# Optimization experiments

Measured on AMD Instinct MI355X. Metric: run time of the kernel, lower is better.

Reference implementation:

```python
import jax, jax.numpy as jnp
import numpy as np

NUM_PROCS = 16
PROC_DIM = 8
SPATIAL_DIM = 3
NUM_LOCS = 500000
NAUG = NUM_PROCS * NUM_LOCS  # 8M augmented rows


def setup_inputs() -> dict:
    key = jax.random.key(0)
    k1, k2, k3, k4 = jax.random.split(key, 4)
    proc_pos = jax.random.normal(k1, (NUM_PROCS, PROC_DIM), dtype=jnp.float32)
    locs_sp = jax.random.normal(k2, (NUM_LOCS, SPATIAL_DIM), dtype=jnp.float32)
    process_ids = jax.random.randint(k3, (NAUG,), 0, NUM_PROCS, dtype=jnp.int64)
    location_ids = jax.random.randint(k4, (NAUG,), 0, NUM_LOCS, dtype=jnp.int64)
    return {
        "proc_pos": proc_pos,
        "locs_sp": locs_sp,
        "process_ids": process_ids,
        "location_ids": location_ids,
    }


def reference(proc_pos, locs_sp, process_ids, location_ids):
    # Fused gather-concat: equivalent to the per-row loop of
    # concat([proc_pos[pid], locs_sp[lid]]) stacked over all augmented rows.
    # [NAUG, PROC_DIM] and [NAUG, SPATIAL_DIM] gathers, then concat on feature axis.
    proc_part = jnp.take(proc_pos, process_ids, axis=0)
    loc_part = jnp.take(locs_sp, location_ids, axis=0)
    locs_augmented = jnp.concatenate([proc_part, loc_part], axis=1)  # [NAUG, PROC_DIM+SPATIAL_DIM]
    return locs_augmented
```

## Files before the change

kernel.cpp:

```cpp
#include <hip/hip_runtime.h>
#include <hip/hip_bf16.h>

#define NUM_PROCS 16
#define PROC_DIM 8
#define SPATIAL_DIM 3
#define ROW_DIM (PROC_DIM + SPATIAL_DIM)
#define BLOCK 256
#define RPT 2
#define ROWS_PER_BLOCK (BLOCK * RPT)

typedef float v4f __attribute__((ext_vector_type(4)));
typedef int   v2i __attribute__((ext_vector_type(2)));

__global__ __launch_bounds__(BLOCK) void gather_concat_kernel(
    const float* __restrict__ proc_pos,
    const float* __restrict__ locs_sp,
    const int*   __restrict__ process_ids,
    const int*   __restrict__ location_ids,
    float* __restrict__ out,
    int naug)
{
    __shared__ float sproc[NUM_PROCS * PROC_DIM];
    __shared__ float s[ROWS_PER_BLOCK * ROW_DIM];

    const int t = threadIdx.x;
    const int block_row0 = blockIdx.x * ROWS_PER_BLOCK;
    const bool full = (block_row0 + ROWS_PER_BLOCK <= naug);

    if (t < NUM_PROCS * PROC_DIM) sproc[t] = proc_pos[t];

    const int r0 = block_row0 + 2 * t;
    v2i pid2, lid2;
    if (full) {
        pid2 = __builtin_nontemporal_load((const v2i*)(process_ids + block_row0) + t);
        lid2 = __builtin_nontemporal_load((const v2i*)(location_ids + block_row0) + t);
    } else {
        pid2.x = (r0     < naug) ? process_ids[r0]     : 0;
        pid2.y = (r0 + 1 < naug) ? process_ids[r0 + 1] : 0;
        lid2.x = (r0     < naug) ? location_ids[r0]     : 0;
        lid2.y = (r0 + 1 < naug) ? location_ids[r0 + 1] : 0;
    }

    const float* lp0 = locs_sp + (size_t)lid2.x * SPATIAL_DIM;
    const float* lp1 = locs_sp + (size_t)lid2.y * SPATIAL_DIM;
    float a0 = lp0[0], a1 = lp0[1], a2 = lp0[2];
    float b0 = lp1[0], b1 = lp1[1], b2 = lp1[2];

    __syncthreads();

    const v4f* pp0 = (const v4f*)(sproc + pid2.x * PROC_DIM);
    const v4f* pp1 = (const v4f*)(sproc + pid2.y * PROC_DIM);
    v4f p00 = pp0[0], p01 = pp0[1];
    v4f p10 = pp1[0], p11 = pp1[1];

    float* d0 = s + (size_t)(2 * t) * ROW_DIM;
    d0[0] = p00.x; d0[1] = p00.y; d0[2] = p00.z; d0[3] = p00.w;
    d0[4] = p01.x; d0[5] = p01.y; d0[6] = p01.z; d0[7] = p01.w;
    d0[8] = a0;    d0[9] = a1;    d0[10] = a2;
    float* d1 = d0 + ROW_DIM;
    d1[0] = p10.x; d1[1] = p10.y; d1[2] = p10.z; d1[3] = p10.w;
    d1[4] = p11.x; d1[5] = p11.y; d1[6] = p11.z; d1[7] = p11.w;
    d1[8] = b0;    d1[9] = b1;    d1[10] = b2;

    __syncthreads();

    const v4f* s4 = (const v4f*)s;
    if (full) {
        v4f* out4 = (v4f*)(out + (size_t)block_row0 * ROW_DIM);
        #pragma unroll
        for (int k = 0; k < (ROWS_PER_BLOCK * ROW_DIM) / 4 / BLOCK; ++k) {
            const int i = t + k * BLOCK;
            __builtin_nontemporal_store(s4[i], out4 + i);
        }
        const int i = t + ((ROWS_PER_BLOCK * ROW_DIM) / 4 / BLOCK) * BLOCK;
        if (i < (ROWS_PER_BLOCK * ROW_DIM) / 4) {
            __builtin_nontemporal_store(s4[i], out4 + i);
        }
    } else {
        const int total_f = (naug - block_row0) * ROW_DIM;
        float* outf = out + (size_t)block_row0 * ROW_DIM;
        for (int i = t; i < total_f; i += BLOCK) {
            outf[i] = s[i];
        }
    }
}

extern "C" void kernel_launch(void* const* d_in, const int* in_sizes, int n_in,
                              void* d_out, int out_size, void* d_ws, size_t ws_size,
                              hipStream_t stream) {
    const float* proc_pos     = (const float*)d_in[0];
    const float* locs_sp      = (const float*)d_in[1];
    const int*   process_ids  = (const int*)d_in[2];
    const int*   location_ids = (const int*)d_in[3];
    float* out = (float*)d_out;

    const int naug = in_sizes[2];
    const int grid = (naug + ROWS_PER_BLOCK - 1) / ROWS_PER_BLOCK;

    gather_concat_kernel<<<grid, BLOCK, 0, stream>>>(
        proc_pos, locs_sp, process_ids, location_ids, out, naug);
}
```

Before: 449.0 us.

## Pack four rows per thread into direct vector stores, dropping shared staging

Each thread now handles four consecutive rows. Four rows span 44 floats, which is exactly eleven 16-byte vectors, so the thread writes its output with 11 nontemporal v4 stores straight from registers. This removes the shared-memory staging buffer and one barrier, and it loads the ids as v4i. The proc table is padded to a stride of 12 in LDS to spread bank accesses. The cost is that each lane's stores are strided by 176 bytes instead of being contiguous across the wavefront, which may hurt write coalescing. The block size is halved.

```diff
diff --git a/kernel.cpp b/kernel.cpp
--- a/kernel.cpp
+++ b/kernel.cpp
@@ -1,16 +1,16 @@
 #include <hip/hip_runtime.h>
-#include <hip/hip_bf16.h>
 
 #define NUM_PROCS 16
 #define PROC_DIM 8
 #define SPATIAL_DIM 3
 #define ROW_DIM (PROC_DIM + SPATIAL_DIM)
-#define BLOCK 256
-#define RPT 2
+#define BLOCK 128
+#define RPT 4
 #define ROWS_PER_BLOCK (BLOCK * RPT)
+#define SPROC_STRIDE 12
 
 typedef float v4f __attribute__((ext_vector_type(4)));
-typedef int   v2i __attribute__((ext_vector_type(2)));
+typedef int   v4i __attribute__((ext_vector_type(4)));
 
 __global__ __launch_bounds__(BLOCK) void gather_concat_kernel(
     const float* __restrict__ proc_pos,
@@ -20,67 +20,80 @@
     float* __restrict__ out,
     int naug)
 {
-    __shared__ float sproc[NUM_PROCS * PROC_DIM];
-    __shared__ float s[ROWS_PER_BLOCK * ROW_DIM];
+    __shared__ float sproc[NUM_PROCS * SPROC_STRIDE];
 
     const int t = threadIdx.x;
     const int block_row0 = blockIdx.x * ROWS_PER_BLOCK;
     const bool full = (block_row0 + ROWS_PER_BLOCK <= naug);
 
-    if (t < NUM_PROCS * PROC_DIM) sproc[t] = proc_pos[t];
-
-    const int r0 = block_row0 + 2 * t;
-    v2i pid2, lid2;
-    if (full) {
-        pid2 = __builtin_nontemporal_load((const v2i*)(process_ids + block_row0) + t);
-        lid2 = __builtin_nontemporal_load((const v2i*)(location_ids + block_row0) + t);
-    } else {
-        pid2.x = (r0     < naug) ? process_ids[r0]     : 0;
-        pid2.y = (r0 + 1 < naug) ? process_ids[r0 + 1] : 0;
-        lid2.x = (r0     < naug) ? location_ids[r0]     : 0;
-        lid2.y = (r0 + 1 < naug) ? location_ids[r0 + 1] : 0;
+    if (t < NUM_PROCS * PROC_DIM) {
+        sproc[(t >> 3) * SPROC_STRIDE + (t & 7)] = proc_pos[t];
     }
 
-    const float* lp0 = locs_sp + (size_t)lid2.x * SPATIAL_DIM;
-    const float* lp1 = locs_sp + (size_t)lid2.y * SPATIAL_DIM;
-    float a0 = lp0[0], a1 = lp0[1], a2 = lp0[2];
-    float b0 = lp1[0], b1 = lp1[1], b2 = lp1[2];
+    const int r0 = block_row0 + RPT * t;
 
-    __syncthreads();
+    if (full) {
+        v4i pid4 = __builtin_nontemporal_load((const v4i*)(process_ids + block_row0) + t);
+        v4i lid4 = __builtin_nontemporal_load((const v4i*)(location_ids + block_row0) + t);
 
-    const v4f* pp0 = (const v4f*)(sproc + pid2.x * PROC_DIM);
-    const v4f* pp1 = (const v4f*)(sproc + pid2.y * PROC_DIM);
-    v4f p00 = pp0[0], p01 = pp0[1];
-    v4f p10 = pp1[0], p11 = pp1[1];
+        const float* l0 = locs_sp + (size_t)lid4.x * SPATIAL_DIM;
+        const float* l1 = locs_sp + (size_t)lid4.y * SPATIAL_DIM;
+        const float* l2 = locs_sp + (size_t)lid4.z * SPATIAL_DIM;
+        const float* l3 = locs_sp + (size_t)lid4.w * SPATIAL_DIM;
+        float a0 = l0[0], a1 = l0[1], a2 = l0[2];
+        float b0 = l1[0], b1 = l1[1], b2 = l1[2];
+        float c0 = l2[0], c1 = l2[1], c2 = l2[2];
+        float e0 = l3[0], e1 = l3[1], e2 = l3[2];
 
-    float* d0 = s + (size_t)(2 * t) * ROW_DIM;
-    d0[0] = p00.x; d0[1] = p00.y; d0[2] = p00.z; d0[3] = p00.w;
-    d0[4] = p01.x; d0[5] = p01.y; d0[6] = p01.z; d0[7] = p01.w;
-    d0[8] = a0;    d0[9] = a1;    d0[10] = a2;
-    float* d1 = d0 + ROW_DIM;
-    d1[0] = p10.x; d1[1] = p10.y; d1[2] = p10.z; d1[3] = p10.w;
-    d1[4] = p11.x; d1[5] = p11.y; d1[6] = p11.z; d1[7] = p11.w;
-    d1[8] = b0;    d1[9] = b1;    d1[10] = b2;
+        __syncthreads();
 
-    __syncthreads();
+        const v4f* P0 = (const v4f*)(sproc + pid4.x * SPROC_STRIDE);
+        const v4f* P1 = (const v4f*)(sproc + pid4.y * SPROC_STRIDE);
+        const v4f* P2 = (const v4f*)(sproc + pid4.z * SPROC_STRIDE);
+        const v4f* P3 = (const v4f*)(sproc + pid4.w * SPROC_STRIDE);
+        v4f p0a = P0[0], p0b = P0[1];
+        v4f p1a = P1[0], p1b = P1[1];
+        v4f p2a = P2[0], p2b = P2[1];
+        v4f p3a = P3[0], p3b = P3[1];
 
-    const v4f* s4 = (const v4f*)s;
-    if (full) {
-        v4f* out4 = (v4f*)(out + (size_t)block_row0 * ROW_DIM);
-        #pragma unroll
-        for (int k = 0; k < (ROWS_PER_BLOCK * ROW_DIM) / 4 / BLOCK; ++k) {
-            const int i = t + k * BLOCK;
-            __builtin_nontemporal_store(s4[i], out4 + i);
-        }
-        const int i = t + ((ROWS_PER_BLOCK * ROW_DIM) / 4 / BLOCK) * BLOCK;
-        if (i < (ROWS_PER_BLOCK * ROW_DIM) / 4) {
-            __builtin_nontemporal_store(s4[i], out4 + i);
-        }
+        v4f w0  = {p0a.x, p0a.y, p0a.z, p0a.w};
+        v4f w1  = {p0b.x, p0b.y, p0b.z, p0b.w};
+        v4f w2  = {a0,    a1,    a2,    p1a.x};
+        v4f w3  = {p1a.y, p1a.z, p1a.w, p1b.x};
+        v4f w4  = {p1b.y, p1b.z, p1b.w, b0   };
+        v4f w5  = {b1,    b2,    p2a.x, p2a.y};
+        v4f w6  = {p2a.z, p2a.w, p2b.x, p2b.y};
+        v4f w7  = {p2b.z, p2b.w, c0,    c1   };
+        v4f w8  = {c2,    p3a.x, p3a.y, p3a.z};
+        v4f w9  = {p3a.w, p3b.x, p3b.y, p3b.z};
+        v4f w10 = {p3b.w, e0,    e1,    e2   };
+
+        v4f* o = (v4f*)(out + (size_t)r0 * ROW_DIM);
+        __builtin_nontemporal_store(w0,  o + 0);
+        __builtin_nontemporal_store(w1,  o + 1);
+        __builtin_nontemporal_store(w2,  o + 2);
+        __builtin_nontemporal_store(w3,  o + 3);
+        __builtin_nontemporal_store(w4,  o + 4);
+        __builtin_nontemporal_store(w5,  o + 5);
+        __builtin_nontemporal_store(w6,  o + 6);
+        __builtin_nontemporal_store(w7,  o + 7);
+        __builtin_nontemporal_store(w8,  o + 8);
+        __builtin_nontemporal_store(w9,  o + 9);
+        __builtin_nontemporal_store(w10, o + 10);
     } else {
-        const int total_f = (naug - block_row0) * ROW_DIM;
-        float* outf = out + (size_t)block_row0 * ROW_DIM;
-        for (int i = t; i < total_f; i += BLOCK) {
-            outf[i] = s[i];
+        __syncthreads();
+        for (int k = 0; k < RPT; ++k) {
+            const int r = r0 + k;
+            if (r < naug) {
+                const int pid = process_ids[r];
+                const int lid = location_ids[r];
+                const float* ps = sproc + pid * SPROC_STRIDE;
+                const float* ls = locs_sp + (size_t)lid * SPATIAL_DIM;
+                float* orow = out + (size_t)r * ROW_DIM;
+                #pragma unroll
+                for (int j = 0; j < PROC_DIM; ++j) orow[j] = ps[j];
+                orow[8] = ls[0]; orow[9] = ls[1]; orow[10] = ls[2];
+            }
         }
     }
 }
```

Result: slower. 1.275 ms (+184.1%).

## Use persistent per-wave tiles with software-pipelined index and gather prefetch

Applied to the files above, without the earlier changes.

Replaces the one-tile-per-block launch with a fixed grid of persistent blocks. Each wave owns its own LDS staging tile, so block-wide barriers are no longer needed inside the loop. Index loads are prefetched two tiles ahead and location gathers one tile ahead to hide global memory latency. The proc table is also padded to a 12-float stride to spread LDS bank access, and leftover rows are handled by a single wave. The cost is more register pressure and a serial tail path.

```diff
diff --git a/kernel.cpp b/kernel.cpp
--- a/kernel.cpp
+++ b/kernel.cpp
@@ -1,13 +1,15 @@
 #include <hip/hip_runtime.h>
-#include <hip/hip_bf16.h>
 
 #define NUM_PROCS 16
 #define PROC_DIM 8
 #define SPATIAL_DIM 3
 #define ROW_DIM (PROC_DIM + SPATIAL_DIM)
 #define BLOCK 256
+#define WAVES_PB (BLOCK / 64)
 #define RPT 2
-#define ROWS_PER_BLOCK (BLOCK * RPT)
+#define TROWS (64 * RPT)
+#define TILE_F (TROWS * ROW_DIM)
+#define SPROC_STRIDE 12
 
 typedef float v4f __attribute__((ext_vector_type(4)));
 typedef int   v2i __attribute__((ext_vector_type(2)));
@@ -20,67 +22,103 @@
     float* __restrict__ out,
     int naug)
 {
-    __shared__ float sproc[NUM_PROCS * PROC_DIM];
-    __shared__ float s[ROWS_PER_BLOCK * ROW_DIM];
+    __shared__ float sproc[NUM_PROCS * SPROC_STRIDE];
+    __shared__ float stage[WAVES_PB][TILE_F];
 
-    const int t = threadIdx.x;
-    const int block_row0 = blockIdx.x * ROWS_PER_BLOCK;
-    const bool full = (block_row0 + ROWS_PER_BLOCK <= naug);
+    const int t    = threadIdx.x;
+    const int wv   = t >> 6;
+    const int lane = t & 63;
 
-    if (t < NUM_PROCS * PROC_DIM) sproc[t] = proc_pos[t];
+    if (t < NUM_PROCS * PROC_DIM)
+        sproc[(t >> 3) * SPROC_STRIDE + (t & 7)] = proc_pos[t];
+    __syncthreads();
 
-    const int r0 = block_row0 + 2 * t;
-    v2i pid2, lid2;
-    if (full) {
-        pid2 = __builtin_nontemporal_load((const v2i*)(process_ids + block_row0) + t);
-        lid2 = __builtin_nontemporal_load((const v2i*)(location_ids + block_row0) + t);
-    } else {
-        pid2.x = (r0     < naug) ? process_ids[r0]     : 0;
-        pid2.y = (r0 + 1 < naug) ? process_ids[r0 + 1] : 0;
-        lid2.x = (r0     < naug) ? location_ids[r0]     : 0;
-        lid2.y = (r0 + 1 < naug) ? location_ids[r0 + 1] : 0;
+    const int WT = naug / TROWS;
+    const int gw = blockIdx.x * WAVES_PB + wv;
+    const int NW = gridDim.x * WAVES_PB;
+
+    float* const sl      = stage[wv];
+    const v4f* const s4  = (const v4f*)sl;
+
+    v2i pidC = {0, 0}, lidC = {0, 0};
+    v2i pidN = {0, 0}, lidN = {0, 0};
+    float ca0=0, ca1=0, ca2=0, cb0=0, cb1=0, cb2=0;
+
+    const int wt0 = gw;
+    const int wt1 = gw + NW;
+    if (wt0 < WT) {
+        pidC = __builtin_nontemporal_load((const v2i*)(process_ids + (size_t)wt0 * TROWS) + lane);
+        lidC = __builtin_nontemporal_load((const v2i*)(location_ids + (size_t)wt0 * TROWS) + lane);
+    }
+    if (wt1 < WT) {
+        pidN = __builtin_nontemporal_load((const v2i*)(process_ids + (size_t)wt1 * TROWS) + lane);
+        lidN = __builtin_nontemporal_load((const v2i*)(location_ids + (size_t)wt1 * TROWS) + lane);
+    }
+    if (wt0 < WT) {
+        const float* l0 = locs_sp + (size_t)lidC.x * SPATIAL_DIM;
+        const float* l1 = locs_sp + (size_t)lidC.y * SPATIAL_DIM;
+        ca0 = l0[0]; ca1 = l0[1]; ca2 = l0[2];
+        cb0 = l1[0]; cb1 = l1[1]; cb2 = l1[2];
     }
 
-    const float* lp0 = locs_sp + (size_t)lid2.x * SPATIAL_DIM;
-    const float* lp1 = locs_sp + (size_t)lid2.y * SPATIAL_DIM;
-    float a0 = lp0[0], a1 = lp0[1], a2 = lp0[2];
-    float b0 = lp1[0], b1 = lp1[1], b2 = lp1[2];
+    for (int wt = wt0; wt < WT; wt += NW) {
+        const int wtn  = wt + NW;
+        const int wtnn = wt + 2 * NW;
 
-    __syncthreads();
+        v2i pidT = {0, 0}, lidT = {0, 0};
+        if (wtnn < WT) {
+            pidT = __builtin_nontemporal_load((const v2i*)(process_ids + (size_t)wtnn * TROWS) + lane);
+            lidT = __builtin_nontemporal_load((const v2i*)(location_ids + (size_t)wtnn * TROWS) + lane);
+        }
 
-    const v4f* pp0 = (const v4f*)(sproc + pid2.x * PROC_DIM);
-    const v4f* pp1 = (const v4f*)(sproc + pid2.y * PROC_DIM);
-    v4f p00 = pp0[0], p01 = pp0[1];
-    v4f p10 = pp1[0], p11 = pp1[1];
+        float na0=0, na1=0, na2=0, nb0=0, nb1=0, nb2=0;
+        if (wtn < WT) {
+            const float* l0 = locs_sp + (size_t)lidN.x * SPATIAL_DIM;
+            const float* l1 = locs_sp + (size_t)lidN.y * SPATIAL_DIM;
+            na0 = l0[0]; na1 = l0[1]; na2 = l0[2];
+            nb0 = l1[0]; nb1 = l1[1]; nb2 = l1[2];
+        }
 
-    float* d0 = s + (size_t)(2 * t) * ROW_DIM;
-    d0[0] = p00.x; d0[1] = p00.y; d0[2] = p00.z; d0[3] = p00.w;
-    d0[4] = p01.x; d0[5] = p01.y; d0[6] = p01.z; d0[7] = p01.w;
-    d0[8] = a0;    d0[9] = a1;    d0[10] = a2;
-    float* d1 = d0 + ROW_DIM;
-    d1[0] = p10.x; d1[1] = p10.y; d1[2] = p10.z; d1[3] = p10.w;
-    d1[4] = p11.x; d1[5] = p11.y; d1[6] = p11.z; d1[7] = p11.w;
-    d1[8] = b0;    d1[9] = b1;    d1[10] = b2;
+        const v4f* P0 = (const v4f*)(sproc + pidC.x * SPROC_STRIDE);
+        const v4f* P1 = (const v4f*)(sproc + pidC.y * SPROC_STRIDE);
+        v4f p00 = P0[0], p01 = P0[1];
+        v4f p10 = P1[0], p11 = P1[1];
+        float* d0 = sl + (size_t)(2 * lane) * ROW_DIM;
+        d0[0] = p00.x; d0[1] = p00.y; d0[2]  = p00.z; d0[3] = p00.w;
+        d0[4] = p01.x; d0[5] = p01.y; d0[6]  = p01.z; d0[7] = p01.w;
+        d0[8] = ca0;   d0[9] = ca1;   d0[10] = ca2;
+        float* d1 = d0 + ROW_DIM;
+        d1[0] = p10.x; d1[1] = p10.y; d1[2]  = p10.z; d1[3] = p10.w;
+        d1[4] = p11.x; d1[5] = p11.y; d1[6]  = p11.z; d1[7] = p11.w;
+        d1[8] = cb0;   d1[9] = cb1;   d1[10] = cb2;
 
-    __syncthreads();
-
-    const v4f* s4 = (const v4f*)s;
-    if (full) {
-        v4f* out4 = (v4f*)(out + (size_t)block_row0 * ROW_DIM);
+        v4f* out4 = (v4f*)(out + (size_t)wt * TILE_F);
         #pragma unroll
-        for (int k = 0; k < (ROWS_PER_BLOCK * ROW_DIM) / 4 / BLOCK; ++k) {
-            const int i = t + k * BLOCK;
+        for (int k = 0; k < 5; ++k) {
+            const int i = lane + k * 64;
             __builtin_nontemporal_store(s4[i], out4 + i);
         }
-        const int i = t + ((ROWS_PER_BLOCK * ROW_DIM) / 4 / BLOCK) * BLOCK;
-        if (i < (ROWS_PER_BLOCK * ROW_DIM) / 4) {
+        if (lane < 32) {
+            const int i = 320 + lane;
             __builtin_nontemporal_store(s4[i], out4 + i);
         }
-    } else {
-        const int total_f = (naug - block_row0) * ROW_DIM;
-        float* outf = out + (size_t)block_row0 * ROW_DIM;
-        for (int i = t; i < total_f; i += BLOCK) {
-            outf[i] = s[i];
+
+        pidC = pidN; lidC = lidN; pidN = pidT; lidN = lidT;
+        ca0 = na0; ca1 = na1; ca2 = na2;
+        cb0 = nb0; cb1 = nb1; cb2 = nb2;
+    }
+
+    const int tail0 = WT * TROWS;
+    if (gw == 0) {
+        for (int r = tail0 + lane; r < naug; r += 64) {
+            const int pid = process_ids[r];
+            const int lid = location_ids[r];
+            const float* ps = sproc + pid * SPROC_STRIDE;
+            const float* ls = locs_sp + (size_t)lid * SPATIAL_DIM;
+            float* orow = out + (size_t)r * ROW_DIM;
+            #pragma unroll
+            for (int j = 0; j < PROC_DIM; ++j) orow[j] = ps[j];
+            orow[8] = ls[0]; orow[9] = ls[1]; orow[10] = ls[2];
         }
     }
 }
@@ -95,7 +133,11 @@
     float* out = (float*)d_out;
 
     const int naug = in_sizes[2];
-    const int grid = (naug + ROWS_PER_BLOCK - 1) / ROWS_PER_BLOCK;
+    const int WT   = naug / TROWS;
+
+    int grid = 1792;
+    if (grid * WAVES_PB > WT) grid = (WT + WAVES_PB - 1) / WAVES_PB;
+    if (grid < 1) grid = 1;
 
     gather_concat_kernel<<<grid, BLOCK, 0, stream>>>(
         proc_pos, locs_sp, process_ids, location_ids, out, naug);
```

New measurement: 461.2 us. 1.03x slower.

## Pad location table to float4 in workspace and gather with vector loads

Applied to the files above, without the earlier changes.

Adds a pre-pass kernel that copies the 3-float location table into a 16-byte-stride padded table in the workspace. The main kernel then reads each location with one 128-bit load instead of three scalar loads. The shared-memory proc table stride also changes to 12 floats, apparently to spread LDS bank accesses. The cost is an extra kernel launch that reads and writes about 8 MB each call, and N_LOCS is hardcoded rather than taken from the input sizes.

```diff
diff --git a/kernel.cpp b/kernel.cpp
--- a/kernel.cpp
+++ b/kernel.cpp
@@ -1,5 +1,4 @@
 #include <hip/hip_runtime.h>
-#include <hip/hip_bf16.h>
 
 #define NUM_PROCS 16
 #define PROC_DIM 8
@@ -8,26 +7,42 @@
 #define BLOCK 256
 #define RPT 2
 #define ROWS_PER_BLOCK (BLOCK * RPT)
+#define SPROC_STRIDE 12
+#define N_LOCS 500000
 
 typedef float v4f __attribute__((ext_vector_type(4)));
 typedef int   v2i __attribute__((ext_vector_type(2)));
 
+__global__ __launch_bounds__(256) void pad_table_kernel(
+    const float* __restrict__ src, float* __restrict__ dst, int n)
+{
+    const int i = blockIdx.x * blockDim.x + threadIdx.x;
+    if (i < n) {
+        const float* s = src + (size_t)i * 3;
+        v4f r; r.x = s[0]; r.y = s[1]; r.z = s[2]; r.w = 0.0f;
+        ((v4f*)dst)[i] = r;
+    }
+}
+
+template<bool PADDED>
 __global__ __launch_bounds__(BLOCK) void gather_concat_kernel(
     const float* __restrict__ proc_pos,
     const float* __restrict__ locs_sp,
+    const float* __restrict__ tab4,
     const int*   __restrict__ process_ids,
     const int*   __restrict__ location_ids,
     float* __restrict__ out,
     int naug)
 {
-    __shared__ float sproc[NUM_PROCS * PROC_DIM];
+    __shared__ float sproc[NUM_PROCS * SPROC_STRIDE];
     __shared__ float s[ROWS_PER_BLOCK * ROW_DIM];
 
     const int t = threadIdx.x;
     const int block_row0 = blockIdx.x * ROWS_PER_BLOCK;
     const bool full = (block_row0 + ROWS_PER_BLOCK <= naug);
 
-    if (t < NUM_PROCS * PROC_DIM) sproc[t] = proc_pos[t];
+    if (t < NUM_PROCS * PROC_DIM)
+        sproc[(t >> 3) * SPROC_STRIDE + (t & 7)] = proc_pos[t];
 
     const int r0 = block_row0 + 2 * t;
     v2i pid2, lid2;
@@ -41,25 +56,33 @@
         lid2.y = (r0 + 1 < naug) ? location_ids[r0 + 1] : 0;
     }
 
-    const float* lp0 = locs_sp + (size_t)lid2.x * SPATIAL_DIM;
-    const float* lp1 = locs_sp + (size_t)lid2.y * SPATIAL_DIM;
-    float a0 = lp0[0], a1 = lp0[1], a2 = lp0[2];
-    float b0 = lp1[0], b1 = lp1[1], b2 = lp1[2];
+    float a0, a1, a2, b0, b1, b2;
+    if (PADDED) {
+        v4f g0 = ((const v4f*)tab4)[lid2.x];
+        v4f g1 = ((const v4f*)tab4)[lid2.y];
+        a0 = g0.x; a1 = g0.y; a2 = g0.z;
+        b0 = g1.x; b1 = g1.y; b2 = g1.z;
+    } else {
+        const float* lp0 = locs_sp + (size_t)lid2.x * SPATIAL_DIM;
+        const float* lp1 = locs_sp + (size_t)lid2.y * SPATIAL_DIM;
+        a0 = lp0[0]; a1 = lp0[1]; a2 = lp0[2];
+        b0 = lp1[0]; b1 = lp1[1]; b2 = lp1[2];
+    }
 
     __syncthreads();
 
-    const v4f* pp0 = (const v4f*)(sproc + pid2.x * PROC_DIM);
-    const v4f* pp1 = (const v4f*)(sproc + pid2.y * PROC_DIM);
+    const v4f* pp0 = (const v4f*)(sproc + pid2.x * SPROC_STRIDE);
+    const v4f* pp1 = (const v4f*)(sproc + pid2.y * SPROC_STRIDE);
     v4f p00 = pp0[0], p01 = pp0[1];
     v4f p10 = pp1[0], p11 = pp1[1];
 
     float* d0 = s + (size_t)(2 * t) * ROW_DIM;
-    d0[0] = p00.x; d0[1] = p00.y; d0[2] = p00.z; d0[3] = p00.w;
-    d0[4] = p01.x; d0[5] = p01.y; d0[6] = p01.z; d0[7] = p01.w;
+    d0[0] = p00.x; d0[1] = p00.y; d0[2]  = p00.z; d0[3] = p00.w;
+    d0[4] = p01.x; d0[5] = p01.y; d0[6]  = p01.z; d0[7] = p01.w;
     d0[8] = a0;    d0[9] = a1;    d0[10] = a2;
     float* d1 = d0 + ROW_DIM;
-    d1[0] = p10.x; d1[1] = p10.y; d1[2] = p10.z; d1[3] = p10.w;
-    d1[4] = p11.x; d1[5] = p11.y; d1[6] = p11.z; d1[7] = p11.w;
+    d1[0] = p10.x; d1[1] = p10.y; d1[2]  = p10.z; d1[3] = p10.w;
+    d1[4] = p11.x; d1[5] = p11.y; d1[6]  = p11.z; d1[7] = p11.w;
     d1[8] = b0;    d1[9] = b1;    d1[10] = b2;
 
     __syncthreads();
@@ -97,6 +120,15 @@
     const int naug = in_sizes[2];
     const int grid = (naug + ROWS_PER_BLOCK - 1) / ROWS_PER_BLOCK;
 
-    gather_concat_kernel<<<grid, BLOCK, 0, stream>>>(
-        proc_pos, locs_sp, process_ids, location_ids, out, naug);
+    const size_t pad_bytes = (size_t)N_LOCS * 4 * sizeof(float);
+    if (d_ws != nullptr && ws_size >= pad_bytes) {
+        float* tab4 = (float*)d_ws;
+        pad_table_kernel<<<(N_LOCS + 255) / 256, 256, 0, stream>>>(
+            locs_sp, tab4, N_LOCS);
+        gather_concat_kernel<true><<<grid, BLOCK, 0, stream>>>(
+            proc_pos, locs_sp, tab4, process_ids, location_ids, out, naug);
+    } else {
+        gather_concat_kernel<false><<<grid, BLOCK, 0, stream>>>(
+            proc_pos, locs_sp, locs_sp, process_ids, location_ids, out, naug);
+    }
 }
```

Result: no change. 457.0 us (+1.8%).
